# Performance work log

Measured on AMD Instinct MI355X. Metric: run time of the kernel, lower is better.

The kernel has to match this reference:

```python
import jax, jax.numpy as jnp
import numpy as np

B, N, D = 256, 64, 128
E, K, T = 8, 2, 80
H = 2 * D  # expert hidden


def setup_inputs() -> dict:
    key = jax.random.key(0)
    ks = jax.random.split(key, 4)
    s = 1.0 / np.sqrt(D)
    return {
        "x": jax.random.normal(ks[0], (B, N, D), dtype=jnp.float32),
        "router_w": jax.random.normal(ks[1], (D, E), dtype=jnp.float32) * s,
        "router_b": jnp.zeros((E,), dtype=jnp.float32),
        "w1": jax.random.normal(ks[2], (E, D, H), dtype=jnp.float32) * s,
        "b1": jnp.zeros((E, H), dtype=jnp.float32),
        "w2": jax.random.normal(ks[3], (E, H, T * 2), dtype=jnp.float32) * (1.0 / np.sqrt(H)),
        "b2": jnp.zeros((E, T * 2), dtype=jnp.float32),
        "A": N,
    }


def reference(x, router_w, router_b, w1, b1, w2, b2, A):
    k = K
    xa = x[:, 1:A]                                   # [B, A-1, D] agents w/o ego
    # --- router: per-sample logits -> softmax -> top-k gates ---
    pooled = xa.mean(axis=1)                         # [B, D]
    logits = pooled @ router_w + router_b            # [B, E]
    probs = jax.nn.softmax(logits, axis=-1)
    topk_probs, topk_idx = jax.lax.top_k(probs, k)   # [B, k]
    # dense gate matrix: sum_k p_k * onehot(idx_k)
    gates = jnp.sum(jax.nn.one_hot(topk_idx, E, dtype=probs.dtype)
                    * topk_probs[..., None], axis=1)  # [B, E]
    # --- experts: per-agent MLP, all experts batched (grouped GEMM form) ---
    h = jax.nn.relu(jnp.einsum('bnd,edh->ebnh', xa, w1) + b1[:, None, None, :])
    out_e = jnp.einsum('ebnh,eho->ebno', h, w2) + b2[:, None, None, :]  # [E,B,A-1,T*2]
    out_e = out_e.reshape(E, out_e.shape[1], out_e.shape[2], T, 2)
    # --- weighted combine (scatter-combine expressed densely) ---
    output = jnp.einsum('be,ebntc->bntc', gates, out_e)  # [B, A-1, T, 2]
    return output
```

## Files before the change

### kernel.cpp

```cpp
#include <hip/hip_runtime.h>
#include <hip/hip_bf16.h>

#define B_   256
#define N_   64
#define D_   128
#define E_   8
#define T_   80
#define H_   256
#define O_   160
#define NTOK 63

typedef __bf16 bf16x8 __attribute__((ext_vector_type(8)));
typedef float  f32x4  __attribute__((ext_vector_type(4)));
typedef unsigned short u16x8 __attribute__((ext_vector_type(8)));
typedef unsigned short u16x4 __attribute__((ext_vector_type(4)));

struct Route { int e0, e1; float g0, g1; };

__device__ __forceinline__ unsigned short f2bf(float f) {
    unsigned int u = __builtin_bit_cast(unsigned int, f);
    u += 0x7FFFu + ((u >> 16) & 1u);
    return (unsigned short)(u >> 16);
}

__global__ __launch_bounds__(256)
void prep_route(const float* __restrict__ x,
                const float* __restrict__ rw,
                const float* __restrict__ rb,
                const float* __restrict__ w1,
                const float* __restrict__ w2,
                unsigned short* __restrict__ w1t,
                unsigned short* __restrict__ w2t,
                Route* __restrict__ rt) {
    __shared__ float smem[1184];
    const int bid = blockIdx.x;
    const int t = threadIdx.x;

    if (bid < 576) {
        const int r  = t >> 3;
        const int c4 = (t & 7) * 4;
        const float* src; unsigned short* dst;
        int src_ld, dst_ld;
        size_t soff, doff;
        if (bid < 256) {
            int e = bid >> 5, rest = bid & 31;
            int dt = rest >> 3, ht = rest & 7;
            soff = ((size_t)e * 128 + dt * 32) * 256 + ht * 32; src_ld = 256;
            doff = ((size_t)e * 256 + ht * 32) * 128 + dt * 32; dst_ld = 128;
            src = w1; dst = w1t;
        } else {
            int id = bid - 256;
            int e = id / 40, rest = id % 40;
            int ht = rest / 5, ot = rest % 5;
            soff = ((size_t)e * 256 + ht * 32) * 160 + ot * 32; src_ld = 160;
            doff = ((size_t)e * 160 + ot * 32) * 256 + ht * 32; dst_ld = 256;
            src = w2; dst = w2t;
        }
        float4 v = *(const float4*)(src + soff + (size_t)r * src_ld + c4);
        smem[r * 33 + c4 + 0] = v.x; smem[r * 33 + c4 + 1] = v.y;
        smem[r * 33 + c4 + 2] = v.z; smem[r * 33 + c4 + 3] = v.w;
        __syncthreads();
        const int c  = t >> 3;
        const int r4 = (t & 7) * 4;
        u16x4 h4;
        h4[0] = f2bf(smem[(r4 + 0) * 33 + c]); h4[1] = f2bf(smem[(r4 + 1) * 33 + c]);
        h4[2] = f2bf(smem[(r4 + 2) * 33 + c]); h4[3] = f2bf(smem[(r4 + 3) * 33 + c]);
        *(u16x4*)(dst + doff + (size_t)c * dst_ld + r4) = h4;
    } else {
        const int b = bid - 576;
        float* part = smem;
        float* pooled = smem + 1024;
        const int c4 = (t & 31) * 4;
        const int rr = t >> 5;
        const float* xb = x + ((size_t)b * N_ + 1) * D_;
        float4 ps = make_float4(0.f, 0.f, 0.f, 0.f);
        for (int row = rr; row < NTOK; row += 8) {
            float4 v = *(const float4*)(xb + (size_t)row * D_ + c4);
            ps.x += v.x; ps.y += v.y; ps.z += v.z; ps.w += v.w;
        }
        *(float4*)&part[rr * 128 + c4] = ps;
        __syncthreads();
        if (t < 128) {
            float s = 0.f;
            #pragma unroll
            for (int i = 0; i < 8; ++i) s += part[i * 128 + t];
            pooled[t] = s * (1.f / 63.f);
        }
        __syncthreads();
        if (t < 64) {
            int e  = t >> 3;
            int dg = t & 7;
            float p = 0.f;
            #pragma unroll
            for (int i = 0; i < 16; ++i)
                p += pooled[dg * 16 + i] * rw[(dg * 16 + i) * E_ + e];
            p += __shfl_xor(p, 1); p += __shfl_xor(p, 2); p += __shfl_xor(p, 4);
            float lg[E_];
            #pragma unroll
            for (int e2 = 0; e2 < E_; ++e2) lg[e2] = __shfl(p, e2 * 8) + rb[e2];
            if (t == 0) {
                float mx = lg[0];
                for (int i = 1; i < E_; ++i) mx = fmaxf(mx, lg[i]);
                float pr[E_]; float den = 0.f;
                for (int i = 0; i < E_; ++i) { pr[i] = expf(lg[i] - mx); den += pr[i]; }
                int i0 = 0;
                for (int i = 1; i < E_; ++i) if (pr[i] > pr[i0]) i0 = i;
                int i1 = (i0 == 0) ? 1 : 0;
                for (int i = 0; i < E_; ++i) if (i != i0 && pr[i] > pr[i1]) i1 = i;
                float inv = 1.f / den;
                Route r; r.e0 = i0; r.e1 = i1;
                r.g0 = pr[i0] * inv; r.g1 = pr[i1] * inv;
                rt[b] = r;
            }
        }
    }
}

__global__ __launch_bounds__(256)
void moe_main(const float* __restrict__ x,
              const float* __restrict__ b1,
              const float* __restrict__ b2,
              const unsigned short* __restrict__ w1t,
              const unsigned short* __restrict__ w2t,
              const Route* __restrict__ rt,
              float* __restrict__ out) {
    const int half = blockIdx.x;
    const int b    = blockIdx.y;
    const int m0   = half * 32;
    const int t    = threadIdx.x;
    const int wv   = t >> 6;
    const int lane = t & 63;
    const int q    = lane >> 4;
    const int r16  = lane & 15;

    __shared__ unsigned short xa_lds[32 * 128];
    __shared__ unsigned short h_lds[32 * 256];

    const Route rr = rt[b];

    {
        int row  = t >> 3;
        int col0 = (t & 7) * 16;
        int n = m0 + row;
        bool valid = (n < NTOK);
        const float* src = x + ((size_t)b * N_ + (1 + n)) * D_ + col0;
        #pragma unroll
        for (int c = 0; c < 4; ++c) {
            float4 v;
            if (valid) v = *(const float4*)(src + c * 4);
            else       v = make_float4(0.f, 0.f, 0.f, 0.f);
            u16x4 h4;
            h4[0] = f2bf(v.x); h4[1] = f2bf(v.y); h4[2] = f2bf(v.z); h4[3] = f2bf(v.w);
            int col = col0 + c * 4;
            *(u16x4*)&xa_lds[row * 128 + (col ^ ((row & 7) << 3))] = h4;
        }
    }

    const f32x4 z4 = {0.f, 0.f, 0.f, 0.f};
    f32x4 acc2[2][3];
    #pragma unroll
    for (int mt = 0; mt < 2; ++mt)
        #pragma unroll
        for (int j = 0; j < 3; ++j) acc2[mt][j] = z4;

    __syncthreads();

    #pragma unroll
    for (int s = 0; s < 2; ++s) {
        const int   e = s ? rr.e1 : rr.e0;
        const float g = s ? rr.g1 : rr.g0;
        const unsigned short* w1e = w1t + (size_t)e * H_ * D_;

        f32x4 acc1[2][4];
        #pragma unroll
        for (int mt = 0; mt < 2; ++mt)
            #pragma unroll
            for (int nt = 0; nt < 4; ++nt) acc1[mt][nt] = z4;

        #pragma unroll
        for (int ks = 0; ks < 4; ++ks) {
            int col0k = ks * 32 + q * 8;
            int row0 = r16, row1 = 16 + r16;
            bf16x8 a0 = __builtin_bit_cast(bf16x8,
                *(const u16x8*)&xa_lds[row0 * 128 + (col0k ^ ((row0 & 7) << 3))]);
            bf16x8 a1 = __builtin_bit_cast(bf16x8,
                *(const u16x8*)&xa_lds[row1 * 128 + (col0k ^ ((row1 & 7) << 3))]);
            #pragma unroll
            for (int nt = 0; nt < 4; ++nt) {
                int col = wv * 64 + nt * 16 + r16;
                bf16x8 bb = __builtin_bit_cast(bf16x8,
                    *(const u16x8*)(w1e + (size_t)col * D_ + col0k));
                acc1[0][nt] = __builtin_amdgcn_mfma_f32_16x16x32_bf16(a0, bb, acc1[0][nt], 0, 0, 0);
                acc1[1][nt] = __builtin_amdgcn_mfma_f32_16x16x32_bf16(a1, bb, acc1[1][nt], 0, 0, 0);
            }
        }

        if (s == 1) __syncthreads();

        float b1v[4];
        #pragma unroll
        for (int nt = 0; nt < 4; ++nt) b1v[nt] = b1[e * H_ + wv * 64 + nt * 16 + r16];
        #pragma unroll
        for (int mt = 0; mt < 2; ++mt)
            #pragma unroll
            for (int nt = 0; nt < 4; ++nt) {
                int col = wv * 64 + nt * 16 + r16;
                #pragma unroll
                for (int rg = 0; rg < 4; ++rg) {
                    int row = mt * 16 + q * 4 + rg;
                    float v = acc1[mt][nt][rg] + b1v[nt];
                    v = fmaxf(v, 0.f) * g;
                    h_lds[row * 256 + (col ^ ((row & 7) << 3))] = f2bf(v);
                }
            }
        __syncthreads();

        const unsigned short* w2e = w2t + (size_t)e * O_ * H_;
        #pragma unroll
        for (int ks = 0; ks < 8; ++ks) {
            int col0k = ks * 32 + q * 8;
            int row0 = r16, row1 = 16 + r16;
            bf16x8 a0 = __builtin_bit_cast(bf16x8,
                *(const u16x8*)&h_lds[row0 * 256 + (col0k ^ ((row0 & 7) << 3))]);
            bf16x8 a1 = __builtin_bit_cast(bf16x8,
                *(const u16x8*)&h_lds[row1 * 256 + (col0k ^ ((row1 & 7) << 3))]);
            #pragma unroll
            for (int j = 0; j < 3; ++j) {
                int nt2 = wv + j * 4;
                if (nt2 < 10) {
                    int col = nt2 * 16 + r16;
                    bf16x8 bb = __builtin_bit_cast(bf16x8,
                        *(const u16x8*)(w2e + (size_t)col * H_ + col0k));
                    acc2[0][j] = __builtin_amdgcn_mfma_f32_16x16x32_bf16(a0, bb, acc2[0][j], 0, 0, 0);
                    acc2[1][j] = __builtin_amdgcn_mfma_f32_16x16x32_bf16(a1, bb, acc2[1][j], 0, 0, 0);
                }
            }
        }
    }

    #pragma unroll
    for (int j = 0; j < 3; ++j) {
        int nt2 = wv + j * 4;
        if (nt2 < 10) {
            int col = nt2 * 16 + r16;
            float bias = rr.g0 * b2[rr.e0 * O_ + col] + rr.g1 * b2[rr.e1 * O_ + col];
            #pragma unroll
            for (int mt = 0; mt < 2; ++mt)
                #pragma unroll
                for (int rg = 0; rg < 4; ++rg) {
                    int row = mt * 16 + q * 4 + rg;
                    int n = m0 + row;
                    if (n < NTOK)
                        out[((size_t)b * NTOK + n) * O_ + col] = acc2[mt][j][rg] + bias;
                }
        }
    }
}

extern "C" void kernel_launch(void* const* d_in, const int* in_sizes, int n_in,
                              void* d_out, int out_size, void* d_ws, size_t ws_size,
                              hipStream_t stream) {
    const float* x  = (const float*)d_in[0];
    const float* rw = (const float*)d_in[1];
    const float* rb = (const float*)d_in[2];
    const float* w1 = (const float*)d_in[3];
    const float* b1 = (const float*)d_in[4];
    const float* w2 = (const float*)d_in[5];
    const float* b2 = (const float*)d_in[6];
    float* out = (float*)d_out;

    unsigned short* w1t = (unsigned short*)d_ws;
    unsigned short* w2t = w1t + (size_t)E_ * H_ * D_;
    Route* rt = (Route*)(w2t + (size_t)E_ * O_ * H_);

    prep_route<<<832, 256, 0, stream>>>(x, rw, rb, w1, w2, w1t, w2t, rt);
    moe_main<<<dim3(2, B_), 256, 0, stream>>>(x, b1, b2, w1t, w2t, rt, out);
}
```

Baseline: 103.8 us.

## Process both routed experts concurrently and reorder prep blocks to route first

The main kernel now computes the first GEMM for both selected experts in one pass, with separate LDS buffers for the two hidden activations. Both second GEMMs then run in a single interleaved loop, removing the serial per-expert loop and one barrier phase. The prep kernel puts routing blocks first and packs two weight-transpose tiles per block, cutting the grid from 832 to 544 blocks. The costs are higher register and LDS use (two accumulator sets, two h buffers) plus a launch_bounds hint of 2 blocks per SM.

```diff
diff --git a/kernel.cpp b/kernel.cpp
--- a/kernel.cpp
+++ b/kernel.cpp
@@ -36,39 +36,9 @@
     const int bid = blockIdx.x;
     const int t = threadIdx.x;
 
-    if (bid < 576) {
-        const int r  = t >> 3;
-        const int c4 = (t & 7) * 4;
-        const float* src; unsigned short* dst;
-        int src_ld, dst_ld;
-        size_t soff, doff;
-        if (bid < 256) {
-            int e = bid >> 5, rest = bid & 31;
-            int dt = rest >> 3, ht = rest & 7;
-            soff = ((size_t)e * 128 + dt * 32) * 256 + ht * 32; src_ld = 256;
-            doff = ((size_t)e * 256 + ht * 32) * 128 + dt * 32; dst_ld = 128;
-            src = w1; dst = w1t;
-        } else {
-            int id = bid - 256;
-            int e = id / 40, rest = id % 40;
-            int ht = rest / 5, ot = rest % 5;
-            soff = ((size_t)e * 256 + ht * 32) * 160 + ot * 32; src_ld = 160;
-            doff = ((size_t)e * 160 + ot * 32) * 256 + ht * 32; dst_ld = 256;
-            src = w2; dst = w2t;
-        }
-        float4 v = *(const float4*)(src + soff + (size_t)r * src_ld + c4);
-        smem[r * 33 + c4 + 0] = v.x; smem[r * 33 + c4 + 1] = v.y;
-        smem[r * 33 + c4 + 2] = v.z; smem[r * 33 + c4 + 3] = v.w;
-        __syncthreads();
-        const int c  = t >> 3;
-        const int r4 = (t & 7) * 4;
-        u16x4 h4;
-        h4[0] = f2bf(smem[(r4 + 0) * 33 + c]); h4[1] = f2bf(smem[(r4 + 1) * 33 + c]);
-        h4[2] = f2bf(smem[(r4 + 2) * 33 + c]); h4[3] = f2bf(smem[(r4 + 3) * 33 + c]);
-        *(u16x4*)(dst + doff + (size_t)c * dst_ld + r4) = h4;
-    } else {
-        const int b = bid - 576;
-        float* part = smem;
+    if (bid < 256) {
+        const int b = bid;
+        float* part   = smem;
         float* pooled = smem + 1024;
         const int c4 = (t & 31) * 4;
         const int rr = t >> 5;
@@ -113,10 +83,45 @@
                 rt[b] = r;
             }
         }
-    }
-}
-
-__global__ __launch_bounds__(256)
+    } else {
+        #pragma unroll
+        for (int ti = 0; ti < 2; ++ti) {
+            const int task = (bid - 256) + ti * 288;
+            if (ti == 1) __syncthreads();
+            const int r  = t >> 3;
+            const int c4 = (t & 7) * 4;
+            const float* src; unsigned short* dst;
+            int src_ld, dst_ld;
+            size_t soff, doff;
+            if (task < 256) {
+                int e = task >> 5, rest = task & 31;
+                int dt = rest >> 3, ht = rest & 7;
+                soff = ((size_t)e * 128 + dt * 32) * 256 + ht * 32; src_ld = 256;
+                doff = ((size_t)e * 256 + ht * 32) * 128 + dt * 32; dst_ld = 128;
+                src = w1; dst = w1t;
+            } else {
+                int id = task - 256;
+                int e = id / 40, rest = id % 40;
+                int ht = rest / 5, ot = rest % 5;
+                soff = ((size_t)e * 256 + ht * 32) * 160 + ot * 32; src_ld = 160;
+                doff = ((size_t)e * 160 + ot * 32) * 256 + ht * 32; dst_ld = 256;
+                src = w2; dst = w2t;
+            }
+            float4 v = *(const float4*)(src + soff + (size_t)r * src_ld + c4);
+            smem[r * 33 + c4 + 0] = v.x; smem[r * 33 + c4 + 1] = v.y;
+            smem[r * 33 + c4 + 2] = v.z; smem[r * 33 + c4 + 3] = v.w;
+            __syncthreads();
+            const int c  = t >> 3;
+            const int r4 = (t & 7) * 4;
+            u16x4 h4;
+            h4[0] = f2bf(smem[(r4 + 0) * 33 + c]); h4[1] = f2bf(smem[(r4 + 1) * 33 + c]);
+            h4[2] = f2bf(smem[(r4 + 2) * 33 + c]); h4[3] = f2bf(smem[(r4 + 3) * 33 + c]);
+            *(u16x4*)(dst + doff + (size_t)c * dst_ld + r4) = h4;
+        }
+    }
+}
+
+__global__ __launch_bounds__(256, 2)
 void moe_main(const float* __restrict__ x,
               const float* __restrict__ b1,
               const float* __restrict__ b2,
@@ -134,9 +139,24 @@
     const int r16  = lane & 15;
 
     __shared__ unsigned short xa_lds[32 * 128];
-    __shared__ unsigned short h_lds[32 * 256];
+    __shared__ unsigned short h0_lds[32 * 256];
+    __shared__ unsigned short h1_lds[32 * 256];
 
     const Route rr = rt[b];
+    const int   e0 = rr.e0, e1 = rr.e1;
+    const float g0 = rr.g0, g1 = rr.g1;
+    const unsigned short* w1e0 = w1t + (size_t)e0 * H_ * D_;
+    const unsigned short* w1e1 = w1t + (size_t)e1 * H_ * D_;
+    const unsigned short* w2e0 = w2t + (size_t)e0 * O_ * H_;
+    const unsigned short* w2e1 = w2t + (size_t)e1 * O_ * H_;
+
+    float b1v0[4], b1v1[4];
+    #pragma unroll
+    for (int nt = 0; nt < 4; ++nt) {
+        int col = wv * 64 + nt * 16 + r16;
+        b1v0[nt] = b1[e0 * H_ + col];
+        b1v1[nt] = b1[e1 * H_ + col];
+    }
 
     {
         int row  = t >> 3;
@@ -157,83 +177,78 @@
     }
 
     const f32x4 z4 = {0.f, 0.f, 0.f, 0.f};
+    f32x4 acc10[2][4], acc11[2][4];
+    #pragma unroll
+    for (int mt = 0; mt < 2; ++mt)
+        #pragma unroll
+        for (int nt = 0; nt < 4; ++nt) { acc10[mt][nt] = z4; acc11[mt][nt] = z4; }
+
+    __syncthreads();
+
+    #pragma unroll
+    for (int ks = 0; ks < 4; ++ks) {
+        int col0k = ks * 32 + q * 8;
+        int row0 = r16, row1 = 16 + r16;
+        bf16x8 a0 = __builtin_bit_cast(bf16x8,
+            *(const u16x8*)&xa_lds[row0 * 128 + (col0k ^ ((row0 & 7) << 3))]);
+        bf16x8 a1 = __builtin_bit_cast(bf16x8,
+            *(const u16x8*)&xa_lds[row1 * 128 + (col0k ^ ((row1 & 7) << 3))]);
+        #pragma unroll
+        for (int nt = 0; nt < 4; ++nt) {
+            size_t woff = (size_t)(wv * 64 + nt * 16 + r16) * D_ + col0k;
+            bf16x8 bb0 = __builtin_bit_cast(bf16x8, *(const u16x8*)(w1e0 + woff));
+            bf16x8 bb1 = __builtin_bit_cast(bf16x8, *(const u16x8*)(w1e1 + woff));
+            acc10[0][nt] = __builtin_amdgcn_mfma_f32_16x16x32_bf16(a0, bb0, acc10[0][nt], 0, 0, 0);
+            acc10[1][nt] = __builtin_amdgcn_mfma_f32_16x16x32_bf16(a1, bb0, acc10[1][nt], 0, 0, 0);
+            acc11[0][nt] = __builtin_amdgcn_mfma_f32_16x16x32_bf16(a0, bb1, acc11[0][nt], 0, 0, 0);
+            acc11[1][nt] = __builtin_amdgcn_mfma_f32_16x16x32_bf16(a1, bb1, acc11[1][nt], 0, 0, 0);
+        }
+    }
+
+    #pragma unroll
+    for (int mt = 0; mt < 2; ++mt)
+        #pragma unroll
+        for (int nt = 0; nt < 4; ++nt) {
+            int col = wv * 64 + nt * 16 + r16;
+            #pragma unroll
+            for (int rg = 0; rg < 4; ++rg) {
+                int row = mt * 16 + q * 4 + rg;
+                int idx = row * 256 + (col ^ ((row & 7) << 3));
+                float v0 = fmaxf(acc10[mt][nt][rg] + b1v0[nt], 0.f) * g0;
+                float v1 = fmaxf(acc11[mt][nt][rg] + b1v1[nt], 0.f) * g1;
+                h0_lds[idx] = f2bf(v0);
+                h1_lds[idx] = f2bf(v1);
+            }
+        }
+    __syncthreads();
+
     f32x4 acc2[2][3];
     #pragma unroll
     for (int mt = 0; mt < 2; ++mt)
         #pragma unroll
         for (int j = 0; j < 3; ++j) acc2[mt][j] = z4;
 
-    __syncthreads();
-
-    #pragma unroll
-    for (int s = 0; s < 2; ++s) {
-        const int   e = s ? rr.e1 : rr.e0;
-        const float g = s ? rr.g1 : rr.g0;
-        const unsigned short* w1e = w1t + (size_t)e * H_ * D_;
-
-        f32x4 acc1[2][4];
-        #pragma unroll
-        for (int mt = 0; mt < 2; ++mt)
-            #pragma unroll
-            for (int nt = 0; nt < 4; ++nt) acc1[mt][nt] = z4;
-
-        #pragma unroll
-        for (int ks = 0; ks < 4; ++ks) {
-            int col0k = ks * 32 + q * 8;
-            int row0 = r16, row1 = 16 + r16;
-            bf16x8 a0 = __builtin_bit_cast(bf16x8,
-                *(const u16x8*)&xa_lds[row0 * 128 + (col0k ^ ((row0 & 7) << 3))]);
-            bf16x8 a1 = __builtin_bit_cast(bf16x8,
-                *(const u16x8*)&xa_lds[row1 * 128 + (col0k ^ ((row1 & 7) << 3))]);
-            #pragma unroll
-            for (int nt = 0; nt < 4; ++nt) {
-                int col = wv * 64 + nt * 16 + r16;
-                bf16x8 bb = __builtin_bit_cast(bf16x8,
-                    *(const u16x8*)(w1e + (size_t)col * D_ + col0k));
-                acc1[0][nt] = __builtin_amdgcn_mfma_f32_16x16x32_bf16(a0, bb, acc1[0][nt], 0, 0, 0);
-                acc1[1][nt] = __builtin_amdgcn_mfma_f32_16x16x32_bf16(a1, bb, acc1[1][nt], 0, 0, 0);
-            }
-        }
-
-        if (s == 1) __syncthreads();
-
-        float b1v[4];
-        #pragma unroll
-        for (int nt = 0; nt < 4; ++nt) b1v[nt] = b1[e * H_ + wv * 64 + nt * 16 + r16];
-        #pragma unroll
-        for (int mt = 0; mt < 2; ++mt)
-            #pragma unroll
-            for (int nt = 0; nt < 4; ++nt) {
-                int col = wv * 64 + nt * 16 + r16;
-                #pragma unroll
-                for (int rg = 0; rg < 4; ++rg) {
-                    int row = mt * 16 + q * 4 + rg;
-                    float v = acc1[mt][nt][rg] + b1v[nt];
-                    v = fmaxf(v, 0.f) * g;
-                    h_lds[row * 256 + (col ^ ((row & 7) << 3))] = f2bf(v);
-                }
-            }
-        __syncthreads();
-
-        const unsigned short* w2e = w2t + (size_t)e * O_ * H_;
-        #pragma unroll
-        for (int ks = 0; ks < 8; ++ks) {
-            int col0k = ks * 32 + q * 8;
-            int row0 = r16, row1 = 16 + r16;
-            bf16x8 a0 = __builtin_bit_cast(bf16x8,
-                *(const u16x8*)&h_lds[row0 * 256 + (col0k ^ ((row0 & 7) << 3))]);
-            bf16x8 a1 = __builtin_bit_cast(bf16x8,
-                *(const u16x8*)&h_lds[row1 * 256 + (col0k ^ ((row1 & 7) << 3))]);
-            #pragma unroll
-            for (int j = 0; j < 3; ++j) {
-                int nt2 = wv + j * 4;
-                if (nt2 < 10) {
-                    int col = nt2 * 16 + r16;
-                    bf16x8 bb = __builtin_bit_cast(bf16x8,
-                        *(const u16x8*)(w2e + (size_t)col * H_ + col0k));
-                    acc2[0][j] = __builtin_amdgcn_mfma_f32_16x16x32_bf16(a0, bb, acc2[0][j], 0, 0, 0);
-                    acc2[1][j] = __builtin_amdgcn_mfma_f32_16x16x32_bf16(a1, bb, acc2[1][j], 0, 0, 0);
-                }
+    #pragma unroll
+    for (int ks = 0; ks < 8; ++ks) {
+        int col0k = ks * 32 + q * 8;
+        int row0 = r16, row1 = 16 + r16;
+        int i0 = row0 * 256 + (col0k ^ ((row0 & 7) << 3));
+        int i1 = row1 * 256 + (col0k ^ ((row1 & 7) << 3));
+        bf16x8 a00 = __builtin_bit_cast(bf16x8, *(const u16x8*)&h0_lds[i0]);
+        bf16x8 a01 = __builtin_bit_cast(bf16x8, *(const u16x8*)&h0_lds[i1]);
+        bf16x8 a10 = __builtin_bit_cast(bf16x8, *(const u16x8*)&h1_lds[i0]);
+        bf16x8 a11 = __builtin_bit_cast(bf16x8, *(const u16x8*)&h1_lds[i1]);
+        #pragma unroll
+        for (int j = 0; j < 3; ++j) {
+            int nt2 = wv + j * 4;
+            if (nt2 < 10) {
+                size_t woff = (size_t)(nt2 * 16 + r16) * H_ + col0k;
+                bf16x8 bb0 = __builtin_bit_cast(bf16x8, *(const u16x8*)(w2e0 + woff));
+                bf16x8 bb1 = __builtin_bit_cast(bf16x8, *(const u16x8*)(w2e1 + woff));
+                acc2[0][j] = __builtin_amdgcn_mfma_f32_16x16x32_bf16(a00, bb0, acc2[0][j], 0, 0, 0);
+                acc2[1][j] = __builtin_amdgcn_mfma_f32_16x16x32_bf16(a01, bb0, acc2[1][j], 0, 0, 0);
+                acc2[0][j] = __builtin_amdgcn_mfma_f32_16x16x32_bf16(a10, bb1, acc2[0][j], 0, 0, 0);
+                acc2[1][j] = __builtin_amdgcn_mfma_f32_16x16x32_bf16(a11, bb1, acc2[1][j], 0, 0, 0);
             }
         }
     }
@@ -243,7 +258,7 @@
         int nt2 = wv + j * 4;
         if (nt2 < 10) {
             int col = nt2 * 16 + r16;
-            float bias = rr.g0 * b2[rr.e0 * O_ + col] + rr.g1 * b2[rr.e1 * O_ + col];
+            float bias = g0 * b2[e0 * O_ + col] + g1 * b2[e1 * O_ + col];
             #pragma unroll
             for (int mt = 0; mt < 2; ++mt)
                 #pragma unroll
@@ -273,6 +288,6 @@
     unsigned short* w2t = w1t + (size_t)E_ * H_ * D_;
     Route* rt = (Route*)(w2t + (size_t)E_ * O_ * H_);
 
-    prep_route<<<832, 256, 0, stream>>>(x, rw, rb, w1, w2, w1t, w2t, rt);
+    prep_route<<<544, 256, 0, stream>>>(x, rw, rb, w1, w2, w1t, w2t, rt);
     moe_main<<<dim3(2, B_), 256, 0, stream>>>(x, b1, b2, w1t, w2t, rt, out);
 }
```

New measurement: 101.4 us. 1.02x faster.
